# Kernel tuning notes

Measured on AMD Instinct MI355X. Metric: run time of the kernel, lower is better.

The kernel has to match this reference:

```python
import jax, jax.numpy as jnp
import numpy as np

L, T, E, D, H, B = 2, 8, 2, 128, 128, 32768
NE = T * E  # total experts per layer = 16


def setup_inputs() -> dict:
    key = jax.random.key(0)
    ks = jax.random.split(key, 8)
    s = 1.0 / np.sqrt(D)
    inputs = jax.random.normal(ks[0], (B, T, D), dtype=jnp.float32)
    w1 = jax.random.uniform(ks[1], (L, NE, D, H), jnp.float32, -s, s)
    b1 = jax.random.uniform(ks[2], (L, NE, H), jnp.float32, -s, s)
    w2 = jax.random.uniform(ks[3], (L, NE, H, H), jnp.float32, -s, s)
    b2 = jax.random.uniform(ks[4], (L, NE, H), jnp.float32, -s, s)
    gate_w = jax.random.uniform(ks[5], (L, T, D, NE), jnp.float32, -s, s)
    gate_b = jax.random.uniform(ks[6], (L, T, NE), jnp.float32, -s, s)
    se = 1.0 / np.sqrt(E)
    sew = jax.random.uniform(ks[7], (L, T, E), jnp.float32, -se, se)
    return {"inputs": inputs, "w1": w1, "b1": b1, "w2": w2, "b2": b2,
            "gate_w": gate_w, "gate_b": gate_b, "sew": sew}


def reference(inputs, w1, b1, w2, b2, gate_w, gate_b, sew):
    x = inputs  # [B, T, D]
    for l in range(L):
        # each task's input feeds its num_task_experts experts
        x_exp = jnp.repeat(x, E, axis=1)  # [B, NE, D]
        h = jax.nn.relu(jnp.einsum('bed,edh->beh', x_exp, w1[l]) + b1[l])
        eo = jax.nn.relu(jnp.einsum('beh,eho->beo', h, w2[l]) + b2[l])  # [B, NE, H]
        # per-task gating over all experts
        gates = jax.nn.softmax(jnp.einsum('btd,tde->bte', x, gate_w[l]) + gate_b[l], axis=-1)  # [B, T, NE]
        fused = jnp.einsum('bte,beh->bth', gates, eo)  # [B, T, H]
        # self-expert residual (num_task_experts > 1 branch)
        eo_r = eo.reshape(eo.shape[0], T, E, -1)  # [B, T, E, H]
        fused = fused + jnp.einsum('te,bteh->bth', sew[l], eo_r)
        x = fused
    return x
```

## Files before the change

kernel.cpp:

```cpp
#include <hip/hip_runtime.h>


typedef float f32x4 __attribute__((ext_vector_type(4)));
typedef _Float16 f16;
typedef f16 f16x8 __attribute__((ext_vector_type(8)));
typedef f16 f16x4 __attribute__((ext_vector_type(4)));

#define MFMA(a, b, c) __builtin_amdgcn_mfma_f32_16x16x32_f16(a, b, c, 0, 0, 0)
#define LOSC (1.0f / 2048.0f)
#define AS1 __attribute__((address_space(1)))
#define AS3 __attribute__((address_space(3)))

__device__ __forceinline__ void split2h(float f, f16& h, f16& l) {
  h = (f16)f;
  l = (f16)((f - (float)h) * 2048.0f);
}

__global__ __launch_bounds__(256) void kxcast(const float* __restrict__ x0,
                                              f16* __restrict__ x0h) {
  size_t i = ((size_t)blockIdx.x * 256 + threadIdx.x) * 8;
  f32x4 f0 = *(const f32x4*)(x0 + i);
  f32x4 f1 = *(const f32x4*)(x0 + i + 4);
  f16x8 v;
#pragma unroll
  for (int z = 0; z < 4; ++z) {
    v[z] = (f16)f0[z];
    v[4 + z] = (f16)f1[z];
  }
  *(f16x8*)(x0h + i) = v;
}

__global__ __launch_bounds__(256) void kxform(
    const float* __restrict__ w1, const float* __restrict__ w2,
    const float* __restrict__ gw, f16* __restrict__ w1T,
    f16* __restrict__ w2T, f16* __restrict__ gwT) {
  int idx = blockIdx.x * 256 + threadIdx.x;
  if (idx < 131072) {
    const float* src = (idx < 65536) ? w1 : w2;
    f16* dst = (idx < 65536) ? w1T : w2T;
    int i = idx & 65535;
    int lane = i & 63;
    int it = (i >> 6) & 7;
    int ks = (i >> 9) & 3;
    int q = i >> 11;
    int g = lane >> 4, le = lane & 15;
    f16x8 vh;
#pragma unroll
    for (int j = 0; j < 8; ++j)
      vh[j] = (f16)src[((size_t)q * 128 + (32 * ks + 8 * g + j)) * 128 + 16 * it + le];
    *(f16x8*)(dst + (size_t)i * 8) = vh;
  } else {
    int i = idx - 131072;
    if (i >= 4096) return;
    int lane = i & 63;
    int ks = (i >> 6) & 3;
    int q = (i >> 8) & 15;
    int g = lane >> 4, le = lane & 15;
    f16x8 vh, vl;
#pragma unroll
    for (int j = 0; j < 8; ++j) {
      float f = gw[((size_t)q * 128 + (32 * ks + 8 * g + j)) * 16 + le];
      f16 h, l;
      split2h(f, h, l);
      vh[j] = h;
      vl[j] = l;
    }
    *(f16x8*)(gwT + (size_t)i * 8) = vh;
    *(f16x8*)(gwT + 32768 + (size_t)i * 8) = vl;
  }
}

__global__ __launch_bounds__(256, 2) void kexp(
    const f16* __restrict__ xs, const f16* __restrict__ w1T,
    const f16* __restrict__ w2T, const float* __restrict__ b1,
    const float* __restrict__ b2, f16* __restrict__ eo, int layer) {
  __shared__ f16 sX[2][8192];
  __shared__ f16 sH[8192];
  __shared__ f16 sEO[8192];
  const int tid = threadIdx.x;
  const int lane = tid & 63;
  const int it2 = tid >> 6;
  const int g = lane >> 4, le = lane & 15;
  const int e = blockIdx.x & 15;
  const int r0 = (blockIdx.x >> 4) * 1024;
  const int te = e >> 1;
  const int lx = layer * 16 + e;

  f16x8 w1r[2][4], w2r[2][4];
#pragma unroll
  for (int i2 = 0; i2 < 2; ++i2)
#pragma unroll
    for (int ks = 0; ks < 4; ++ks) {
      size_t fb = ((size_t)((lx * 4 + ks) * 8 + 2 * it2 + i2) * 64 + lane) * 8;
      w1r[i2][ks] = *(const f16x8*)(w1T + fb);
      w2r[i2][ks] = *(const f16x8*)(w2T + fb);
    }
  f32x4 b1v[2], b2v[2];
#pragma unroll
  for (int i2 = 0; i2 < 2; ++i2) {
    b1v[i2] = *(const f32x4*)(b1 + lx * 128 + 32 * it2 + 16 * i2 + 4 * g);
    b2v[i2] = *(const f32x4*)(b2 + lx * 128 + 32 * it2 + 16 * i2 + 4 * g);
  }

  auto stage_gl = [&](int buf, int tile) {
#pragma unroll
    for (int i = 0; i < 4; ++i) {
      int row = 16 * it2 + 4 * i + (lane >> 4);
      int gc = lane & 15;
      const f16* src = xs + ((size_t)(r0 + tile * 64 + row) * 8 + te) * 128 +
                       (gc ^ (row & 7)) * 8;
      f16* dst = &sX[buf][(16 * it2 + 4 * i) * 128];
      __builtin_amdgcn_global_load_lds((const AS1 void*)src, (AS3 void*)dst,
                                       16, 0, 0);
    }
  };
  auto eo_flush = [&](int tile) {
#pragma unroll
    for (int i = 0; i < 4; ++i) {
      int slot = i * 256 + tid;
      int row = slot >> 4, c = slot & 15;
      f16x8 v = *(const f16x8*)(&sEO[row * 128 + 8 * (c ^ (row & 7))]);
      *(f16x8*)(eo + ((size_t)e * 32768 + (r0 + tile * 64 + row)) * 128 + 8 * c) = v;
    }
  };

  stage_gl(0, 0);
  __syncthreads();

  for (int tile = 0; tile < 16; ++tile) {
    const int b = tile & 1;
    if (tile < 15) stage_gl(b ^ 1, tile + 1);
    if (tile > 0) eo_flush(tile - 1);
    {
      f32x4 a[2][4];
#pragma unroll
      for (int i2 = 0; i2 < 2; ++i2)
#pragma unroll
        for (int j = 0; j < 4; ++j) a[i2][j] = f32x4{0.f, 0.f, 0.f, 0.f};
#pragma unroll
      for (int ks = 0; ks < 4; ++ks)
#pragma unroll
        for (int j = 0; j < 4; ++j) {
          int brow = 16 * j + le;
          f16x8 bf = *(const f16x8*)(&sX[b][brow * 128 + 8 * ((4 * ks + g) ^ (brow & 7))]);
#pragma unroll
          for (int i2 = 0; i2 < 2; ++i2)
            a[i2][j] = MFMA(w1r[i2][ks], bf, a[i2][j]);
        }
#pragma unroll
      for (int i2 = 0; i2 < 2; ++i2)
#pragma unroll
        for (int j = 0; j < 4; ++j) {
          int brow = 16 * j + le;
          f16x4 hv;
#pragma unroll
          for (int r = 0; r < 4; ++r)
            hv[r] = (f16)fmaxf(a[i2][j][r] + b1v[i2][r], 0.f);
          *(f16x4*)(&sH[brow * 128 + 8 * ((4 * it2 + 2 * i2 + (g >> 1)) ^ (brow & 7)) +
                        4 * (g & 1)]) = hv;
        }
    }
    __syncthreads();
    {
      f32x4 a[2][4];
#pragma unroll
      for (int i2 = 0; i2 < 2; ++i2)
#pragma unroll
        for (int j = 0; j < 4; ++j) a[i2][j] = f32x4{0.f, 0.f, 0.f, 0.f};
#pragma unroll
      for (int ks = 0; ks < 4; ++ks)
#pragma unroll
        for (int j = 0; j < 4; ++j) {
          int brow = 16 * j + le;
          f16x8 bf = *(const f16x8*)(&sH[brow * 128 + 8 * ((4 * ks + g) ^ (brow & 7))]);
#pragma unroll
          for (int i2 = 0; i2 < 2; ++i2)
            a[i2][j] = MFMA(w2r[i2][ks], bf, a[i2][j]);
        }
#pragma unroll
      for (int i2 = 0; i2 < 2; ++i2)
#pragma unroll
        for (int j = 0; j < 4; ++j) {
          int brow = 16 * j + le;
          f16x4 ev;
#pragma unroll
          for (int r = 0; r < 4; ++r)
            ev[r] = (f16)fmaxf(a[i2][j][r] + b2v[i2][r], 0.f);
          *(f16x4*)(&sEO[brow * 128 + 8 * ((4 * it2 + 2 * i2 + (g >> 1)) ^ (brow & 7)) +
                         4 * (g & 1)]) = ev;
        }
    }
    __syncthreads();
  }
  eo_flush(15);
}

__global__ __launch_bounds__(512, 4) void kmix(
    const f16* __restrict__ xs, const f16* __restrict__ gwT,
    const float* __restrict__ gb, const float* __restrict__ sw,
    const f16* __restrict__ eo, f16* __restrict__ x1out,
    float* __restrict__ fout, int layer) {
  __shared__ float sG[8 * 16 * 32];
  const int tid = threadIdx.x;
  const int lane = tid & 63;
  const int t = tid >> 6;
  const int g = lane >> 4, le = lane & 15;
  const int r0 = blockIdx.x * 32;
  const int lt = layer * 8 + t;

  {
    f32x4 l1[2], l2[2];
#pragma unroll
    for (int j = 0; j < 2; ++j) {
      l1[j] = f32x4{0.f, 0.f, 0.f, 0.f};
      l2[j] = f32x4{0.f, 0.f, 0.f, 0.f};
    }
#pragma unroll
    for (int ks = 0; ks < 4; ++ks) {
      size_t fb = ((size_t)(lt * 4 + ks) * 64 + lane) * 8;
      f16x8 ah = *(const f16x8*)(gwT + fb);
      f16x8 al = *(const f16x8*)(gwT + 32768 + fb);
#pragma unroll
      for (int j = 0; j < 2; ++j) {
        f16x8 bf = *(const f16x8*)(xs + ((size_t)(r0 + 16 * j + le) * 8 + t) * 128 +
                                   32 * ks + 8 * g);
        l1[j] = MFMA(ah, bf, l1[j]);
        l2[j] = MFMA(al, bf, l2[j]);
      }
    }
#pragma unroll
    for (int j = 0; j < 2; ++j) {
      float zb[4];
#pragma unroll
      for (int r = 0; r < 4; ++r)
        zb[r] = l1[j][r] + l2[j][r] * LOSC + gb[lt * 16 + 4 * g + r];
      float m4 = fmaxf(fmaxf(zb[0], zb[1]), fmaxf(zb[2], zb[3]));
      m4 = fmaxf(m4, __shfl_xor(m4, 16, 64));
      m4 = fmaxf(m4, __shfl_xor(m4, 32, 64));
      float p4[4], s4 = 0.f;
#pragma unroll
      for (int r = 0; r < 4; ++r) {
        p4[r] = __expf(zb[r] - m4);
        s4 += p4[r];
      }
      s4 += __shfl_xor(s4, 16, 64);
      s4 += __shfl_xor(s4, 32, 64);
      float inv = 1.f / s4;
#pragma unroll
      for (int r = 0; r < 4; ++r)
        sG[(t * 16 + 4 * g + r) * 32 + 16 * j + le] = p4[r] * inv;
    }
  }
  __syncthreads();

  const int lrow = tid >> 4;
  const int grow = r0 + lrow;
  const int cq = (tid & 15) * 8;
  f32x4 am[8][2];
#pragma unroll
  for (int tt = 0; tt < 8; ++tt)
#pragma unroll
    for (int k = 0; k < 2; ++k) am[tt][k] = f32x4{0.f, 0.f, 0.f, 0.f};

  for (int ee = 0; ee < 16; ++ee) {
    const int tte = ee >> 1, eh = ee & 1;
    f16x8 ev = *(const f16x8*)(eo + ((size_t)ee * 32768 + grow) * 128 + cq);
    float evf[8];
#pragma unroll
    for (int z = 0; z < 8; ++z) evf[z] = (float)ev[z];
    float ssew = sw[(layer * 8 + tte) * 2 + eh];
#pragma unroll
    for (int tt = 0; tt < 8; ++tt) {
      float coef = sG[(tt * 16 + ee) * 32 + lrow] + (tt == tte ? ssew : 0.f);
#pragma unroll
      for (int z = 0; z < 8; ++z)
        am[tt][z >> 2][z & 3] = fmaf(coef, evf[z], am[tt][z >> 2][z & 3]);
    }
  }
#pragma unroll
  for (int tt = 0; tt < 8; ++tt) {
    size_t off = ((size_t)grow * 8 + tt) * 128 + cq;
    if (layer == 0) {
      f16x8 hv;
#pragma unroll
      for (int z = 0; z < 8; ++z) hv[z] = (f16)am[tt][z >> 2][z & 3];
      *(f16x8*)(x1out + off) = hv;
    } else {
      *(f32x4*)(fout + off) = am[tt][0];
      *(f32x4*)(fout + off + 4) = am[tt][1];
    }
  }
}

extern "C" void kernel_launch(void* const* d_in, const int* in_sizes, int n_in,
                              void* d_out, int out_size, void* d_ws, size_t ws_size,
                              hipStream_t stream) {
  const float* x0 = (const float*)d_in[0];
  const float* w1 = (const float*)d_in[1];
  const float* b1 = (const float*)d_in[2];
  const float* w2 = (const float*)d_in[3];
  const float* b2 = (const float*)d_in[4];
  const float* gw = (const float*)d_in[5];
  const float* gb = (const float*)d_in[6];
  const float* sw = (const float*)d_in[7];

  f16* w1T = (f16*)d_ws;
  f16* w2T = (f16*)((char*)d_ws + 1048576);
  f16* gwT = (f16*)((char*)d_ws + 2097152);
  f16* x0h = (f16*)((char*)d_ws + 4194304);
  f16* x1h = (f16*)((char*)d_ws + 71303168);
  f16* eo = (f16*)((char*)d_ws + 138412032);
  float* out = (float*)d_out;

  kxform<<<528, 256, 0, stream>>>(w1, w2, gw, w1T, w2T, gwT);
  kxcast<<<16384, 256, 0, stream>>>(x0, x0h);

  kexp<<<512, 256, 0, stream>>>(x0h, w1T, w2T, b1, b2, eo, 0);
  kmix<<<1024, 512, 0, stream>>>(x0h, gwT, gb, sw, eo, x1h, nullptr, 0);
  kexp<<<512, 256, 0, stream>>>(x1h, w1T, w2T, b1, b2, eo, 1);
  kmix<<<1024, 512, 0, stream>>>(x1h, gwT, gb, sw, eo, nullptr, out, 1);
}
```

Measured before the change: 275.7 us.

## Retile expert MLP waves to 64x32 blocks and merge prep kernels

Each wave in the expert kernel now computes 64 output features by 32 rows instead of 32 features by 64 rows. The B fragment loaded from LDS is reused across four MFMAs instead of two, which halves LDS reads per MFMA. The cost is doubling the weight fragments held in registers, and empty asm statements are added to keep those registers from being rematerialized. Separately, the weight-transform and input-cast kernels are merged into one launch to save launch overhead.

```diff
diff --git a/kernel.cpp b/kernel.cpp
--- a/kernel.cpp
+++ b/kernel.cpp
@@ -16,25 +16,27 @@
   l = (f16)((f - (float)h) * 2048.0f);
 }
 
-__global__ __launch_bounds__(256) void kxcast(const float* __restrict__ x0,
-                                              f16* __restrict__ x0h) {
-  size_t i = ((size_t)blockIdx.x * 256 + threadIdx.x) * 8;
-  f32x4 f0 = *(const f32x4*)(x0 + i);
-  f32x4 f1 = *(const f32x4*)(x0 + i + 4);
-  f16x8 v;
-#pragma unroll
-  for (int z = 0; z < 4; ++z) {
-    v[z] = (f16)f0[z];
-    v[4 + z] = (f16)f1[z];
-  }
-  *(f16x8*)(x0h + i) = v;
-}
-
-__global__ __launch_bounds__(256) void kxform(
-    const float* __restrict__ w1, const float* __restrict__ w2,
-    const float* __restrict__ gw, f16* __restrict__ w1T,
-    f16* __restrict__ w2T, f16* __restrict__ gwT) {
-  int idx = blockIdx.x * 256 + threadIdx.x;
+__global__ __launch_bounds__(256) void kprep(
+    const float* __restrict__ x0, const float* __restrict__ w1,
+    const float* __restrict__ w2, const float* __restrict__ gw,
+    f16* __restrict__ x0h, f16* __restrict__ w1T, f16* __restrict__ w2T,
+    f16* __restrict__ gwT) {
+  int bid = blockIdx.x;
+  int tid = threadIdx.x;
+  if (bid < 16384) {
+    size_t i = ((size_t)bid * 256 + tid) * 8;
+    f32x4 f0 = *(const f32x4*)(x0 + i);
+    f32x4 f1 = *(const f32x4*)(x0 + i + 4);
+    f16x8 v;
+#pragma unroll
+    for (int z = 0; z < 4; ++z) {
+      v[z] = (f16)f0[z];
+      v[4 + z] = (f16)f1[z];
+    }
+    *(f16x8*)(x0h + i) = v;
+    return;
+  }
+  int idx = (bid - 16384) * 256 + tid;
   if (idx < 131072) {
     const float* src = (idx < 65536) ? w1 : w2;
     f16* dst = (idx < 65536) ? w1T : w2T;
@@ -51,7 +53,6 @@
     *(f16x8*)(dst + (size_t)i * 8) = vh;
   } else {
     int i = idx - 131072;
-    if (i >= 4096) return;
     int lane = i & 63;
     int ks = (i >> 6) & 3;
     int q = (i >> 8) & 15;
@@ -79,37 +80,38 @@
   __shared__ f16 sEO[8192];
   const int tid = threadIdx.x;
   const int lane = tid & 63;
-  const int it2 = tid >> 6;
+  const int wave = tid >> 6;
+  const int jh = wave & 1, oh = wave >> 1;
   const int g = lane >> 4, le = lane & 15;
   const int e = blockIdx.x & 15;
   const int r0 = (blockIdx.x >> 4) * 1024;
   const int te = e >> 1;
   const int lx = layer * 16 + e;
 
-  f16x8 w1r[2][4], w2r[2][4];
-#pragma unroll
-  for (int i2 = 0; i2 < 2; ++i2)
+  f16x8 w1r[4][4], w2r[4][4];
+#pragma unroll
+  for (int it = 0; it < 4; ++it)
 #pragma unroll
     for (int ks = 0; ks < 4; ++ks) {
-      size_t fb = ((size_t)((lx * 4 + ks) * 8 + 2 * it2 + i2) * 64 + lane) * 8;
-      w1r[i2][ks] = *(const f16x8*)(w1T + fb);
-      w2r[i2][ks] = *(const f16x8*)(w2T + fb);
-    }
-  f32x4 b1v[2], b2v[2];
-#pragma unroll
-  for (int i2 = 0; i2 < 2; ++i2) {
-    b1v[i2] = *(const f32x4*)(b1 + lx * 128 + 32 * it2 + 16 * i2 + 4 * g);
-    b2v[i2] = *(const f32x4*)(b2 + lx * 128 + 32 * it2 + 16 * i2 + 4 * g);
+      size_t fb = ((size_t)((lx * 4 + ks) * 8 + 4 * oh + it) * 64 + lane) * 8;
+      w1r[it][ks] = *(const f16x8*)(w1T + fb);
+      w2r[it][ks] = *(const f16x8*)(w2T + fb);
+    }
+  f32x4 b1v[4], b2v[4];
+#pragma unroll
+  for (int it = 0; it < 4; ++it) {
+    b1v[it] = *(const f32x4*)(b1 + lx * 128 + 64 * oh + 16 * it + 4 * g);
+    b2v[it] = *(const f32x4*)(b2 + lx * 128 + 64 * oh + 16 * it + 4 * g);
   }
 
   auto stage_gl = [&](int buf, int tile) {
 #pragma unroll
     for (int i = 0; i < 4; ++i) {
-      int row = 16 * it2 + 4 * i + (lane >> 4);
+      int row = 16 * wave + 4 * i + (lane >> 4);
       int gc = lane & 15;
       const f16* src = xs + ((size_t)(r0 + tile * 64 + row) * 8 + te) * 128 +
                        (gc ^ (row & 7)) * 8;
-      f16* dst = &sX[buf][(16 * it2 + 4 * i) * 128];
+      f16* dst = &sX[buf][(16 * wave + 4 * i) * 128];
       __builtin_amdgcn_global_load_lds((const AS1 void*)src, (AS3 void*)dst,
                                        16, 0, 0);
     }
@@ -132,64 +134,71 @@
     if (tile < 15) stage_gl(b ^ 1, tile + 1);
     if (tile > 0) eo_flush(tile - 1);
     {
-      f32x4 a[2][4];
-#pragma unroll
-      for (int i2 = 0; i2 < 2; ++i2)
-#pragma unroll
-        for (int j = 0; j < 4; ++j) a[i2][j] = f32x4{0.f, 0.f, 0.f, 0.f};
+      f32x4 a[4][2];
+#pragma unroll
+      for (int it = 0; it < 4; ++it)
+#pragma unroll
+        for (int j2 = 0; j2 < 2; ++j2) a[it][j2] = f32x4{0.f, 0.f, 0.f, 0.f};
 #pragma unroll
       for (int ks = 0; ks < 4; ++ks)
 #pragma unroll
-        for (int j = 0; j < 4; ++j) {
-          int brow = 16 * j + le;
+        for (int j2 = 0; j2 < 2; ++j2) {
+          int brow = 32 * jh + 16 * j2 + le;
           f16x8 bf = *(const f16x8*)(&sX[b][brow * 128 + 8 * ((4 * ks + g) ^ (brow & 7))]);
 #pragma unroll
-          for (int i2 = 0; i2 < 2; ++i2)
-            a[i2][j] = MFMA(w1r[i2][ks], bf, a[i2][j]);
+          for (int it = 0; it < 4; ++it)
+            a[it][j2] = MFMA(w1r[it][ks], bf, a[it][j2]);
         }
 #pragma unroll
-      for (int i2 = 0; i2 < 2; ++i2)
-#pragma unroll
-        for (int j = 0; j < 4; ++j) {
-          int brow = 16 * j + le;
+      for (int it = 0; it < 4; ++it)
+#pragma unroll
+        for (int j2 = 0; j2 < 2; ++j2) {
+          int brow = 32 * jh + 16 * j2 + le;
           f16x4 hv;
 #pragma unroll
           for (int r = 0; r < 4; ++r)
-            hv[r] = (f16)fmaxf(a[i2][j][r] + b1v[i2][r], 0.f);
-          *(f16x4*)(&sH[brow * 128 + 8 * ((4 * it2 + 2 * i2 + (g >> 1)) ^ (brow & 7)) +
-                        4 * (g & 1)]) = hv;
+            hv[r] = (f16)fmaxf(a[it][j2][r] + b1v[it][r], 0.f);
+          int gran = 8 * oh + 2 * it + (g >> 1);
+          *(f16x4*)(&sH[brow * 128 + 8 * (gran ^ (brow & 7)) + 4 * (g & 1)]) = hv;
         }
     }
     __syncthreads();
     {
-      f32x4 a[2][4];
-#pragma unroll
-      for (int i2 = 0; i2 < 2; ++i2)
-#pragma unroll
-        for (int j = 0; j < 4; ++j) a[i2][j] = f32x4{0.f, 0.f, 0.f, 0.f};
+      f32x4 a[4][2];
+#pragma unroll
+      for (int it = 0; it < 4; ++it)
+#pragma unroll
+        for (int j2 = 0; j2 < 2; ++j2) a[it][j2] = f32x4{0.f, 0.f, 0.f, 0.f};
 #pragma unroll
       for (int ks = 0; ks < 4; ++ks)
 #pragma unroll
-        for (int j = 0; j < 4; ++j) {
-          int brow = 16 * j + le;
+        for (int j2 = 0; j2 < 2; ++j2) {
+          int brow = 32 * jh + 16 * j2 + le;
           f16x8 bf = *(const f16x8*)(&sH[brow * 128 + 8 * ((4 * ks + g) ^ (brow & 7))]);
 #pragma unroll
-          for (int i2 = 0; i2 < 2; ++i2)
-            a[i2][j] = MFMA(w2r[i2][ks], bf, a[i2][j]);
+          for (int it = 0; it < 4; ++it)
+            a[it][j2] = MFMA(w2r[it][ks], bf, a[it][j2]);
         }
 #pragma unroll
-      for (int i2 = 0; i2 < 2; ++i2)
-#pragma unroll
-        for (int j = 0; j < 4; ++j) {
-          int brow = 16 * j + le;
+      for (int it = 0; it < 4; ++it)
+#pragma unroll
+        for (int j2 = 0; j2 < 2; ++j2) {
+          int brow = 32 * jh + 16 * j2 + le;
           f16x4 ev;
 #pragma unroll
           for (int r = 0; r < 4; ++r)
-            ev[r] = (f16)fmaxf(a[i2][j][r] + b2v[i2][r], 0.f);
-          *(f16x4*)(&sEO[brow * 128 + 8 * ((4 * it2 + 2 * i2 + (g >> 1)) ^ (brow & 7)) +
-                         4 * (g & 1)]) = ev;
+            ev[r] = (f16)fmaxf(a[it][j2][r] + b2v[it][r], 0.f);
+          int gran = 8 * oh + 2 * it + (g >> 1);
+          *(f16x4*)(&sEO[brow * 128 + 8 * (gran ^ (brow & 7)) + 4 * (g & 1)]) = ev;
         }
     }
+#pragma unroll
+    for (int it = 0; it < 4; ++it)
+#pragma unroll
+      for (int ks = 0; ks < 4; ++ks) {
+        asm volatile("" : "+v"(w1r[it][ks]));
+        asm volatile("" : "+v"(w2r[it][ks]));
+      }
     __syncthreads();
   }
   eo_flush(15);
@@ -312,8 +321,7 @@
   f16* eo = (f16*)((char*)d_ws + 138412032);
   float* out = (float*)d_out;
 
-  kxform<<<528, 256, 0, stream>>>(w1, w2, gw, w1T, w2T, gwT);
-  kxcast<<<16384, 256, 0, stream>>>(x0, x0h);
+  kprep<<<16912, 256, 0, stream>>>(x0, w1, w2, gw, x0h, w1T, w2T, gwT);
 
   kexp<<<512, 256, 0, stream>>>(x0h, w1T, w2T, b1, b2, eo, 0);
   kmix<<<1024, 512, 0, stream>>>(x0h, gwT, gb, sw, eo, x1h, nullptr, 0);
```

Result: faster. 269.7 us (median of 2 runs) (-2.2%).
